# Kernel tuning notes

Measured on AMD Instinct MI355X. Metric: run time of the kernel, lower is better.

## Reference

```python
import jax, jax.numpy as jnp
import numpy as np


def setup_inputs() -> dict:
    key = jax.random.key(0)
    k1, k2, k3 = jax.random.split(key, 3)
    B, S, D, H = 16, 4096, 512, 512
    inp = jax.random.normal(k1, (B, S, D), dtype=jnp.float32)
    # torch nn.Linear(D, 3*H): weight (3H, D), bias (3H,)
    W = jax.random.normal(k2, (3 * H, D), dtype=jnp.float32) * (1.0 / np.sqrt(D))
    b = jax.random.normal(k3, (3 * H,), dtype=jnp.float32) * 0.01
    return {"inp": inp, "W": W, "b": b}


def _forget_mult(z, f):
    # z, f: (B, S, H). h_t = f_t*z_t + (1-f_t)*h_{t-1}, h_{-1}=0 (hid=None)
    zt = jnp.swapaxes(z, 0, 1)  # (S, B, H)
    ft = jnp.swapaxes(f, 0, 1)
    h0 = jnp.zeros(z.shape[0:1] + z.shape[2:3], dtype=z.dtype)  # (B, H)

    def step(h, zf):
        zi, fi = zf
        h = fi * zi + (1.0 - fi) * h
        return h, h

    _, hs = jax.lax.scan(step, h0, (zt, ft))
    return jnp.swapaxes(hs, 0, 1)  # (B, S, H)


def reference(inp, W, b):
    # QRNNLayer forward: window=1, output_gate=True, batch_first=True,
    # backward=False, zoneout=0, hid=None.
    y = jnp.einsum('bsd,hd->bsh', inp, W) + b  # (B, S, 3H)
    z_gate, f_gate, o_gate = jnp.split(y, 3, axis=2)
    z_gate = jnp.tanh(z_gate)
    f_gate = jax.nn.sigmoid(f_gate)
    c_gate = _forget_mult(z_gate, f_gate)
    output = jax.nn.sigmoid(o_gate) * c_gate
    return output, c_gate[:, -1]
```

## Files before the change

### kernel.cpp

```cpp
#include <hip/hip_runtime.h>
#include <stdint.h>

#define Bdim 16
#define Sdim 4096
#define Hdim 512
#define Mdim (Bdim*Sdim)
#define N3   (3*Hdim)
#define Kdim 512
#define NCHUNK 64
#define CLEN  (Sdim/NCHUNK)

typedef __bf16 bf16;
typedef __bf16 bf16x4 __attribute__((ext_vector_type(4)));
typedef __bf16 bf16x8 __attribute__((ext_vector_type(8)));
typedef float  f32x4  __attribute__((ext_vector_type(4)));
typedef _Float16 f16;
typedef _Float16 f16x4 __attribute__((ext_vector_type(4)));
typedef _Float16 f16x8 __attribute__((ext_vector_type(8)));

__device__ __forceinline__ void gload_lds16(const void* g, void* l) {
  __builtin_amdgcn_global_load_lds(
      (const __attribute__((address_space(1))) uint32_t*)g,
      (__attribute__((address_space(3))) uint32_t*)l, 16, 0, 0);
}

__global__ void __launch_bounds__(256) cvt_kernel(const float4* __restrict__ in,
                                                  bf16x4* __restrict__ out, int n4) {
  int i = blockIdx.x * blockDim.x + threadIdx.x;
  if (i >= n4) return;
  float4 v = in[i];
  bf16x4 o;
  o.x = (bf16)v.x; o.y = (bf16)v.y; o.z = (bf16)v.z; o.w = (bf16)v.w;
  out[i] = o;
}

#define BM 256
#define BN 256
#define BKT 64
#define NKT (Kdim/BKT)

__device__ __forceinline__ bf16x8 lds_ld(const char* p) { return *(const bf16x8*)p; }

__device__ __forceinline__ void read_af(bf16x8 (&d)[4][2], const char* Lb, uint32_t base,
                                        uint32_t swk0, uint32_t swk1, int mh) {
  #pragma unroll
  for (int i = 0; i < 4; ++i) {
    d[i][0] = lds_ld(Lb + base + mh * 8192 + i * 2048 + swk0);
    d[i][1] = lds_ld(Lb + base + mh * 8192 + i * 2048 + swk1);
  }
}
__device__ __forceinline__ void read_bf(bf16x8 (&d)[2][2], const char* Lb, uint32_t base,
                                        uint32_t swk0, uint32_t swk1, int nh) {
  #pragma unroll
  for (int j = 0; j < 2; ++j) {
    d[j][0] = lds_ld(Lb + base + nh * 4096 + j * 2048 + swk0);
    d[j][1] = lds_ld(Lb + base + nh * 4096 + j * 2048 + swk1);
  }
}
__device__ __forceinline__ void chunk16(f32x4 (&acc)[8][4], const bf16x8 (&a)[4][2],
                                        const bf16x8 (&b)[2][2], int mb, int nb) {
  __builtin_amdgcn_s_setprio(1);
  #pragma unroll
  for (int i = 0; i < 4; ++i)
    #pragma unroll
    for (int j = 0; j < 2; ++j)
      #pragma unroll
      for (int kk = 0; kk < 2; ++kk)
        acc[mb + i][nb + j] =
            __builtin_amdgcn_mfma_f32_16x16x32_bf16(a[i][kk], b[j][kk], acc[mb + i][nb + j], 0, 0, 0);
  __builtin_amdgcn_s_setprio(0);
}

template <int H>
__device__ __forceinline__ void stage_half(const bf16* Ag, const bf16* Bg, char* lds,
                                           uint32_t so0, uint32_t wbase) {
  if constexpr (H <= 4 * NKT - 1) {
    constexpr int th = H >> 2, ss = H & 3;
    constexpr uint32_t goff = (uint32_t)((ss >> 1) * 128 * Kdim + th * BKT);
    constexpr uint32_t lbase = (uint32_t)((th & 1) * 65536 + (ss & 1) * 32768 + (ss >> 1) * 16384);
    const bf16* gp = (ss & 1) ? Bg : Ag;
    gload_lds16(gp + goff + so0,         lds + lbase + wbase);
    gload_lds16(gp + goff + so0 + 32768, lds + lbase + 8192 + wbase);
  }
}

#define BAR()   __builtin_amdgcn_s_barrier()
#define LGKM0() do { asm volatile("s_waitcnt lgkmcnt(0)" ::: "memory"); \
                     __builtin_amdgcn_sched_barrier(0); } while (0)

template <int T>
__device__ __forceinline__ void ktile(char* lds, f32x4 (&acc)[8][4],
    bf16x8 (&af0)[4][2], bf16x8 (&af1)[4][2], bf16x8 (&bf0)[2][2], bf16x8 (&bf1)[2][2],
    const bf16* Ag, const bf16* Bg, uint32_t so0, uint32_t wbase,
    uint32_t aBase, uint32_t bBase, uint32_t swk0, uint32_t swk1) {
  const char* Lb = lds + (T & 1) * 65536;
  read_af(af0, Lb, aBase, swk0, swk1, 0);
  read_bf(bf0, Lb, bBase, swk0, swk1, 0);
  stage_half<4 * T + 6>(Ag, Bg, lds, so0, wbase);
  BAR(); LGKM0();
  chunk16(acc, af0, bf0, 0, 0);
  BAR();
  read_af(af1, Lb, aBase, swk0, swk1, 1);
  stage_half<4 * T + 7>(Ag, Bg, lds, so0, wbase);
  BAR(); LGKM0();
  chunk16(acc, af1, bf0, 4, 0);
  BAR();
  read_bf(bf1, Lb, bBase, swk0, swk1, 1);
  stage_half<4 * T + 8>(Ag, Bg, lds, so0, wbase);
  BAR(); LGKM0();
  chunk16(acc, af1, bf1, 4, 2);
  BAR();
  stage_half<4 * T + 9>(Ag, Bg, lds, so0, wbase);
  BAR(); LGKM0();
  chunk16(acc, af0, bf1, 0, 2);
  if constexpr (T <= NKT - 3) {
    asm volatile("s_waitcnt vmcnt(4)" ::: "memory");
  } else if constexpr (T == NKT - 2) {
    asm volatile("s_waitcnt vmcnt(0)" ::: "memory");
  }
  BAR();
}

__global__ void __launch_bounds__(512, 2) gemm_act_kernel(
    const bf16* __restrict__ A, const bf16* __restrict__ Wb,
    const float* __restrict__ bias,
    f16* __restrict__ zbuf, f16* __restrict__ fbuf, f16* __restrict__ ogbuf) {
  __shared__ char lds[131072];
  const int tid  = threadIdx.x;
  const int wid  = tid >> 6;
  const int lane = tid & 63;
  const int wr = wid >> 2, wc = wid & 3;
  const int bid = blockIdx.x;
  const int wg  = (bid & 7) * 192 + (bid >> 3);
  const int mt = wg / (N3 / BN);
  const int nt = wg % (N3 / BN);
  const int row0 = mt * BM;

  const bf16* Ag = A  + (size_t)row0 * Kdim;
  const bf16* Bg = Wb + (size_t)(nt * BN) * Kdim;

  const uint32_t r0   = tid >> 3;
  const uint32_t slot = tid & 7;
  const uint32_t so0  = r0 * Kdim + ((slot ^ (r0 & 7)) << 3);
  const uint32_t wbase = (uint32_t)(wid * 1024);
  const uint32_t kslot = lane >> 4;
  const uint32_t swk0 = ((kslot)     ^ (uint32_t)(lane & 7)) << 4;
  const uint32_t swk1 = ((4 + kslot) ^ (uint32_t)(lane & 7)) << 4;
  const uint32_t aBase = (uint32_t)((wr * 128 + (lane & 15)) * 128);
  const uint32_t bBase = (uint32_t)(32768 + (wc * 64 + (lane & 15)) * 128);

  f32x4 acc[8][4];
  #pragma unroll
  for (int m = 0; m < 8; ++m)
    #pragma unroll
    for (int n = 0; n < 4; ++n)
      acc[m][n] = (f32x4){0.f, 0.f, 0.f, 0.f};
  bf16x8 af0[4][2], af1[4][2], bf0[2][2], bf1[2][2];

  stage_half<0>(Ag, Bg, lds, so0, wbase);
  stage_half<1>(Ag, Bg, lds, so0, wbase);
  stage_half<2>(Ag, Bg, lds, so0, wbase);
  stage_half<3>(Ag, Bg, lds, so0, wbase);
  stage_half<4>(Ag, Bg, lds, so0, wbase);
  stage_half<5>(Ag, Bg, lds, so0, wbase);
  asm volatile("s_waitcnt vmcnt(4)" ::: "memory");
  BAR();

  ktile<0>(lds, acc, af0, af1, bf0, bf1, Ag, Bg, so0, wbase, aBase, bBase, swk0, swk1);
  ktile<1>(lds, acc, af0, af1, bf0, bf1, Ag, Bg, so0, wbase, aBase, bBase, swk0, swk1);
  ktile<2>(lds, acc, af0, af1, bf0, bf1, Ag, Bg, so0, wbase, aBase, bBase, swk0, swk1);
  ktile<3>(lds, acc, af0, af1, bf0, bf1, Ag, Bg, so0, wbase, aBase, bBase, swk0, swk1);
  ktile<4>(lds, acc, af0, af1, bf0, bf1, Ag, Bg, so0, wbase, aBase, bBase, swk0, swk1);
  ktile<5>(lds, acc, af0, af1, bf0, bf1, Ag, Bg, so0, wbase, aBase, bBase, swk0, swk1);
  ktile<6>(lds, acc, af0, af1, bf0, bf1, Ag, Bg, so0, wbase, aBase, bBase, swk0, swk1);
  ktile<7>(lds, acc, af0, af1, bf0, bf1, Ag, Bg, so0, wbase, aBase, bBase, swk0, swk1);

  __syncthreads();

  const int gate = nt >> 1;
  const int cb   = (nt & 1) * 256;
  f16* dst = (gate == 0) ? zbuf : ((gate == 1) ? fbuf : ogbuf);
  float bv[4];
  #pragma unroll
  for (int n = 0; n < 4; ++n)
    bv[n] = bias[gate * Hdim + cb + wc * 64 + n * 16 + (lane & 15)];

  #pragma unroll
  for (int m = 0; m < 8; ++m) {
    #pragma unroll
    for (int n = 0; n < 4; ++n) {
      int col = wc * 64 + n * 16 + (lane & 15);
      #pragma unroll
      for (int r = 0; r < 4; ++r) {
        int row = wr * 128 + m * 16 + (lane >> 4) * 4 + r;
        float y = acc[m][n][r] + bv[n];
        float v;
        if (gate == 0) {
          float e = __expf(2.f * y);
          v = 1.f - 2.f / (e + 1.f);
        } else {
          v = 1.f / (1.f + __expf(-y));
        }
        uint32_t byte = (uint32_t)(row * 512 + col * 2) ^ ((uint32_t)(row & 7) << 4);
        *(f16*)(lds + byte) = (f16)v;
      }
    }
  }
  __syncthreads();
  #pragma unroll
  for (int j = 0; j < 16; ++j) {
    int c = j * 512 + tid;
    int row = c >> 5, col8 = c & 31;
    uint32_t byte = (uint32_t)(row * 512 + col8 * 16) ^ ((uint32_t)(row & 7) << 4);
    f16x8 v = *(const f16x8*)(lds + byte);
    *(f16x8*)&dst[(size_t)(row0 + row) * Hdim + cb + col8 * 8] = v;
  }
}

__global__ void __launch_bounds__(256) scanA_kernel(const f16x4* __restrict__ z4,
                                                    const f16x4* __restrict__ f4,
                                                    float* __restrict__ Pb,
                                                    float* __restrict__ Qb) {
  int u  = blockIdx.x * blockDim.x + threadIdx.x;
  int hq = u & 127;
  int bc = u >> 7;
  int b  = bc & (Bdim - 1);
  int c  = bc >> 4;
  size_t base = ((size_t)(b * Sdim + c * CLEN)) * 128 + hq;
  float P[4] = {1.f, 1.f, 1.f, 1.f}, Q[4] = {0.f, 0.f, 0.f, 0.f};
  #pragma unroll 4
  for (int s = 0; s < CLEN; ++s) {
    f16x4 fv = f4[base], zv = z4[base];
    #pragma unroll
    for (int j = 0; j < 4; ++j) {
      float f = (float)fv[j];
      Q[j] += f * ((float)zv[j] - Q[j]);
      P[j] *= (1.f - f);
    }
    base += 128;
  }
  int outi = ((c * Bdim + b) << 9) + hq * 4;
  *(float4*)&Pb[outi] = make_float4(P[0], P[1], P[2], P[3]);
  *(float4*)&Qb[outi] = make_float4(Q[0], Q[1], Q[2], Q[3]);
}

__global__ void __launch_bounds__(256) scanB_kernel(const float* __restrict__ Pb,
                                                    const float* __restrict__ Qb,
                                                    float* __restrict__ hin,
                                                    float* __restrict__ c_last) {
  int t = blockIdx.x * blockDim.x + threadIdx.x;
  int h = t & (Hdim - 1), b = t >> 9;
  float hs = 0.f;
  #pragma unroll 8
  for (int c = 0; c < NCHUNK; ++c) {
    hin[c * (Bdim * Hdim) + t] = hs;
    int u = ((c * Bdim + b) << 9) + h;
    hs = Pb[u] * hs + Qb[u];
  }
  c_last[t] = hs;
}

__global__ void __launch_bounds__(256) scanC_kernel(const f16x4* __restrict__ z4,
                                                    const f16x4* __restrict__ f4,
                                                    const f16x4* __restrict__ og4,
                                                    const float* __restrict__ hin,
                                                    float4* __restrict__ out4) {
  int u  = blockIdx.x * blockDim.x + threadIdx.x;
  int hq = u & 127;
  int bc = u >> 7;
  int b  = bc & (Bdim - 1);
  int c  = bc >> 4;
  float4 hv = *(const float4*)&hin[c * (Bdim * Hdim) + b * Hdim + hq * 4];
  float h[4] = {hv.x, hv.y, hv.z, hv.w};
  size_t base = ((size_t)(b * Sdim + c * CLEN)) * 128 + hq;
  #pragma unroll 4
  for (int s = 0; s < CLEN; ++s) {
    f16x4 fv = f4[base], zv = z4[base], ov = og4[base];
    float4 o;
    #pragma unroll
    for (int j = 0; j < 4; ++j) {
      h[j] += (float)fv[j] * ((float)zv[j] - h[j]);
    }
    o.x = (float)ov[0] * h[0]; o.y = (float)ov[1] * h[1];
    o.z = (float)ov[2] * h[2]; o.w = (float)ov[3] * h[3];
    out4[base] = o;
    base += 128;
  }
}

extern "C" void kernel_launch(void* const* d_in, const int* in_sizes, int n_in,
                              void* d_out, int out_size, void* d_ws, size_t ws_size,
                              hipStream_t stream) {
  const float* inp  = (const float*)d_in[0];
  const float* W    = (const float*)d_in[1];
  const float* bias = (const float*)d_in[2];
  float* out = (float*)d_out;

  char* ws = (char*)d_ws;
  bf16* Abf = (bf16*)(ws);
  bf16* Wbf = (bf16*)(ws + 67108864);
  f16*  zh  = (f16*) (ws + 68681728);
  f16*  fh  = (f16*) (ws + 135790592);
  f16*  ogh = (f16*) (ws + 202899456);
  float* Pb = (float*)(ws + 270008320);
  float* Qb = (float*)(ws + 272105472);
  float* hin= (float*)(ws + 274202624);

  {
    int n4 = (Mdim * Kdim) / 4;
    cvt_kernel<<<n4 / 256, 256, 0, stream>>>((const float4*)inp, (bf16x4*)Abf, n4);
  }
  {
    int n4 = (N3 * Kdim) / 4;
    cvt_kernel<<<n4 / 256, 256, 0, stream>>>((const float4*)W, (bf16x4*)Wbf, n4);
  }
  gemm_act_kernel<<<(Mdim / BM) * (N3 / BN), 512, 0, stream>>>(Abf, Wbf, bias,
                                                               zh, fh, ogh);
  scanA_kernel<<<(NCHUNK * Bdim * 128) / 256, 256, 0, stream>>>(
      (const f16x4*)zh, (const f16x4*)fh, Pb, Qb);
  scanB_kernel<<<(Bdim * Hdim) / 256, 256, 0, stream>>>(Pb, Qb, hin,
                                                        out + (size_t)Mdim * Hdim);
  scanC_kernel<<<(NCHUNK * Bdim * 128) / 256, 256, 0, stream>>>(
      (const f16x4*)zh, (const f16x4*)fh, (const f16x4*)ogh, hin, (float4*)out);
}
```

Baseline: 308.4 us.

## Make GEMM persistent with next-tile prefetch overlapped with epilogue

The GEMM+activation kernel becomes persistent: 256 workgroups each loop over 6 output tiles instead of launching one workgroup per tile. While the epilogue of the current tile runs, the first K-tile stages of the next tile are loaded into the free LDS buffer, and the epilogue is split into two halves so it fits in the other half of LDS. This hides global-load latency and launch/prologue cost, but occupancy drops to one block per CU, the tile-order swizzle is removed, and the waitcnt accounting is fragile.

```diff
diff --git a/kernel.cpp b/kernel.cpp
--- a/kernel.cpp
+++ b/kernel.cpp
@@ -82,6 +82,14 @@
     gload_lds16(gp + goff + so0,         lds + lbase + wbase);
     gload_lds16(gp + goff + so0 + 32768, lds + lbase + 8192 + wbase);
   }
+}
+__device__ __forceinline__ void stage_halfR(int th, int ss, const bf16* Ap, const bf16* Bp,
+                                            char* lds, uint32_t so0, uint32_t wbase) {
+  uint32_t goff  = (uint32_t)((ss >> 1) * 128 * Kdim + th * BKT);
+  uint32_t lbase = (uint32_t)((th & 1) * 65536 + (ss & 1) * 32768 + (ss >> 1) * 16384);
+  const bf16* gp = (ss & 1) ? Bp : Ap;
+  gload_lds16(gp + goff + so0,         lds + lbase + wbase);
+  gload_lds16(gp + goff + so0 + 32768, lds + lbase + 8192 + wbase);
 }
 
 #define BAR()   __builtin_amdgcn_s_barrier()
@@ -131,13 +139,6 @@
   const int lane = tid & 63;
   const int wr = wid >> 2, wc = wid & 3;
   const int bid = blockIdx.x;
-  const int wg  = (bid & 7) * 192 + (bid >> 3);
-  const int mt = wg / (N3 / BN);
-  const int nt = wg % (N3 / BN);
-  const int row0 = mt * BM;
-
-  const bf16* Ag = A  + (size_t)row0 * Kdim;
-  const bf16* Bg = Wb + (size_t)(nt * BN) * Kdim;
 
   const uint32_t r0   = tid >> 3;
   const uint32_t slot = tid & 7;
@@ -149,71 +150,117 @@
   const uint32_t aBase = (uint32_t)((wr * 128 + (lane & 15)) * 128);
   const uint32_t bBase = (uint32_t)(32768 + (wc * 64 + (lane & 15)) * 128);
 
-  f32x4 acc[8][4];
-  #pragma unroll
-  for (int m = 0; m < 8; ++m)
+  bf16x8 af0[4][2], af1[4][2], bf0[2][2], bf1[2][2];
+
+  {
+    uint32_t g0 = (uint32_t)bid;
+    uint32_t mt0 = g0 / 6;
+    uint32_t nt0 = g0 - 6 * mt0;
+    const bf16* Ag = A  + (size_t)mt0 * BM * Kdim;
+    const bf16* Bg = Wb + (size_t)nt0 * BN * Kdim;
+    stage_half<0>(Ag, Bg, lds, so0, wbase);
+    stage_half<1>(Ag, Bg, lds, so0, wbase);
+    stage_half<2>(Ag, Bg, lds, so0, wbase);
+    stage_half<3>(Ag, Bg, lds, so0, wbase);
+    stage_half<4>(Ag, Bg, lds, so0, wbase);
+    stage_half<5>(Ag, Bg, lds, so0, wbase);
+    asm volatile("s_waitcnt vmcnt(4)" ::: "memory");
+    BAR();
+  }
+
+  #pragma unroll 1
+  for (int it = 0; it < 6; ++it) {
+    const uint32_t g  = (uint32_t)(it * 256 + bid);
+    const uint32_t mt = g / 6;
+    const uint32_t nt = g - 6 * mt;
+    const int row0 = (int)mt * BM;
+    const bf16* Ag = A  + (size_t)mt * BM * Kdim;
+    const bf16* Bg = Wb + (size_t)nt * BN * Kdim;
+
+    f32x4 acc[8][4];
+    #pragma unroll
+    for (int m = 0; m < 8; ++m)
+      #pragma unroll
+      for (int n = 0; n < 4; ++n)
+        acc[m][n] = (f32x4){0.f, 0.f, 0.f, 0.f};
+
+    ktile<0>(lds, acc, af0, af1, bf0, bf1, Ag, Bg, so0, wbase, aBase, bBase, swk0, swk1);
+    ktile<1>(lds, acc, af0, af1, bf0, bf1, Ag, Bg, so0, wbase, aBase, bBase, swk0, swk1);
+    ktile<2>(lds, acc, af0, af1, bf0, bf1, Ag, Bg, so0, wbase, aBase, bBase, swk0, swk1);
+    ktile<3>(lds, acc, af0, af1, bf0, bf1, Ag, Bg, so0, wbase, aBase, bBase, swk0, swk1);
+    ktile<4>(lds, acc, af0, af1, bf0, bf1, Ag, Bg, so0, wbase, aBase, bBase, swk0, swk1);
+    ktile<5>(lds, acc, af0, af1, bf0, bf1, Ag, Bg, so0, wbase, aBase, bBase, swk0, swk1);
+    ktile<6>(lds, acc, af0, af1, bf0, bf1, Ag, Bg, so0, wbase, aBase, bBase, swk0, swk1);
+    ktile<7>(lds, acc, af0, af1, bf0, bf1, Ag, Bg, so0, wbase, aBase, bBase, swk0, swk1);
+
+    const int gate = (int)(nt >> 1);
+    const int cbn  = (int)(nt & 1) * 256;
+    f16* dst = (gate == 0) ? zbuf : ((gate == 1) ? fbuf : ogbuf);
+    float bv[4];
     #pragma unroll
     for (int n = 0; n < 4; ++n)
-      acc[m][n] = (f32x4){0.f, 0.f, 0.f, 0.f};
-  bf16x8 af0[4][2], af1[4][2], bf0[2][2], bf1[2][2];
-
-  stage_half<0>(Ag, Bg, lds, so0, wbase);
-  stage_half<1>(Ag, Bg, lds, so0, wbase);
-  stage_half<2>(Ag, Bg, lds, so0, wbase);
-  stage_half<3>(Ag, Bg, lds, so0, wbase);
-  stage_half<4>(Ag, Bg, lds, so0, wbase);
-  stage_half<5>(Ag, Bg, lds, so0, wbase);
-  asm volatile("s_waitcnt vmcnt(4)" ::: "memory");
-  BAR();
-
-  ktile<0>(lds, acc, af0, af1, bf0, bf1, Ag, Bg, so0, wbase, aBase, bBase, swk0, swk1);
-  ktile<1>(lds, acc, af0, af1, bf0, bf1, Ag, Bg, so0, wbase, aBase, bBase, swk0, swk1);
-  ktile<2>(lds, acc, af0, af1, bf0, bf1, Ag, Bg, so0, wbase, aBase, bBase, swk0, swk1);
-  ktile<3>(lds, acc, af0, af1, bf0, bf1, Ag, Bg, so0, wbase, aBase, bBase, swk0, swk1);
-  ktile<4>(lds, acc, af0, af1, bf0, bf1, Ag, Bg, so0, wbase, aBase, bBase, swk0, swk1);
-  ktile<5>(lds, acc, af0, af1, bf0, bf1, Ag, Bg, so0, wbase, aBase, bBase, swk0, swk1);
-  ktile<6>(lds, acc, af0, af1, bf0, bf1, Ag, Bg, so0, wbase, aBase, bBase, swk0, swk1);
-  ktile<7>(lds, acc, af0, af1, bf0, bf1, Ag, Bg, so0, wbase, aBase, bBase, swk0, swk1);
-
-  __syncthreads();
-
-  const int gate = nt >> 1;
-  const int cb   = (nt & 1) * 256;
-  f16* dst = (gate == 0) ? zbuf : ((gate == 1) ? fbuf : ogbuf);
-  float bv[4];
-  #pragma unroll
-  for (int n = 0; n < 4; ++n)
-    bv[n] = bias[gate * Hdim + cb + wc * 64 + n * 16 + (lane & 15)];
-
-  #pragma unroll
-  for (int m = 0; m < 8; ++m) {
-    #pragma unroll
-    for (int n = 0; n < 4; ++n) {
-      int col = wc * 64 + n * 16 + (lane & 15);
+      bv[n] = bias[gate * Hdim + cbn + wc * 64 + n * 16 + (lane & 15)];
+
+    const bool stageNext = (it < 5);
+    const bf16* AgN = A; const bf16* BgN = Wb;
+    if (stageNext) {
+      uint32_t gN  = g + 256;
+      uint32_t mtN = gN / 6;
+      uint32_t ntN = gN - 6 * mtN;
+      AgN = A  + (size_t)mtN * BM * Kdim;
+      BgN = Wb + (size_t)ntN * BN * Kdim;
+      stage_halfR(0, 0, AgN, BgN, lds, so0, wbase);
+      stage_halfR(0, 1, AgN, BgN, lds, so0, wbase);
+      stage_halfR(0, 2, AgN, BgN, lds, so0, wbase);
+      stage_halfR(0, 3, AgN, BgN, lds, so0, wbase);
+    }
+
+    char* scr = lds + 65536;
+    #pragma unroll
+    for (int R = 0; R < 2; ++R) {
       #pragma unroll
-      for (int r = 0; r < 4; ++r) {
-        int row = wr * 128 + m * 16 + (lane >> 4) * 4 + r;
-        float y = acc[m][n][r] + bv[n];
-        float v;
-        if (gate == 0) {
-          float e = __expf(2.f * y);
-          v = 1.f - 2.f / (e + 1.f);
-        } else {
-          v = 1.f / (1.f + __expf(-y));
+      for (int m4 = 0; m4 < 4; ++m4) {
+        const int m = R * 4 + m4;
+        #pragma unroll
+        for (int n = 0; n < 4; ++n) {
+          int col = wc * 64 + n * 16 + (lane & 15);
+          #pragma unroll
+          for (int r = 0; r < 4; ++r) {
+            int Lrow = wr * 64 + m4 * 16 + (lane >> 4) * 4 + r;
+            float y = acc[m][n][r] + bv[n];
+            float v;
+            if (gate == 0) {
+              float e = __expf(2.f * y);
+              v = 1.f - 2.f / (e + 1.f);
+            } else {
+              v = 1.f / (1.f + __expf(-y));
+            }
+            uint32_t byte = (uint32_t)(Lrow * 512 + col * 2) ^ ((uint32_t)(Lrow & 7) << 4);
+            *(f16*)(scr + byte) = (f16)v;
+          }
         }
-        uint32_t byte = (uint32_t)(row * 512 + col * 2) ^ ((uint32_t)(row & 7) << 4);
-        *(f16*)(lds + byte) = (f16)v;
       }
-    }
-  }
-  __syncthreads();
-  #pragma unroll
-  for (int j = 0; j < 16; ++j) {
-    int c = j * 512 + tid;
-    int row = c >> 5, col8 = c & 31;
-    uint32_t byte = (uint32_t)(row * 512 + col8 * 16) ^ ((uint32_t)(row & 7) << 4);
-    f16x8 v = *(const f16x8*)(lds + byte);
-    *(f16x8*)&dst[(size_t)(row0 + row) * Hdim + cb + col8 * 8] = v;
+      asm volatile("s_waitcnt lgkmcnt(0)" ::: "memory");
+      BAR();
+      #pragma unroll
+      for (int j = 0; j < 8; ++j) {
+        int c = j * 512 + tid;
+        int Lrow = c >> 5, col8 = c & 31;
+        uint32_t byte = (uint32_t)(Lrow * 512 + col8 * 16) ^ ((uint32_t)(Lrow & 7) << 4);
+        f16x8 v = *(const f16x8*)(scr + byte);
+        int G = (Lrow >> 6) * 128 + R * 64 + (Lrow & 63);
+        *(f16x8*)&dst[(size_t)(row0 + G) * Hdim + cbn + col8 * 8] = v;
+      }
+      asm volatile("s_waitcnt lgkmcnt(0)" ::: "memory");
+      BAR();
+    }
+
+    if (stageNext) {
+      stage_halfR(1, 0, AgN, BgN, lds, so0, wbase);
+      stage_halfR(1, 1, AgN, BgN, lds, so0, wbase);
+      asm volatile("s_waitcnt vmcnt(20)" ::: "memory");
+      BAR();
+    }
   }
 }
 
@@ -314,8 +361,7 @@
     int n4 = (N3 * Kdim) / 4;
     cvt_kernel<<<n4 / 256, 256, 0, stream>>>((const float4*)W, (bf16x4*)Wbf, n4);
   }
-  gemm_act_kernel<<<(Mdim / BM) * (N3 / BN), 512, 0, stream>>>(Abf, Wbf, bias,
-                                                               zh, fh, ogh);
+  gemm_act_kernel<<<256, 512, 0, stream>>>(Abf, Wbf, bias, zh, fh, ogh);
   scanA_kernel<<<(NCHUNK * Bdim * 128) / 256, 256, 0, stream>>>(
       (const f16x4*)zh, (const f16x4*)fh, Pb, Qb);
   scanB_kernel<<<(Bdim * Hdim) / 256, 256, 0, stream>>>(Pb, Qb, hin,
```

Result: slower. 399.2 us (+29.5%).
